# Performance work log

Measured on AMD Instinct MI355X. Metric: run time of the kernel, lower is better.

Reference implementation:

```python
import jax, jax.numpy as jnp
import numpy as np

N = 100000
MUL = 16


def _build_cg():
    # Real-basis Clebsch-Gordan (Wigner-3j-style) coefficients, shape (2l1+1, 2l2+1, 2lo+1),
    # each normalized to unit Frobenius norm per output component (e3nn component normalization).
    eps = np.zeros((3, 3, 3), np.float32)
    for a, b, c in [(0, 1, 2), (1, 2, 0), (2, 0, 1)]:
        eps[a, b, c] = 1.0
        eps[a, c, b] = -1.0
    s2 = np.float32(1.0 / np.sqrt(2.0))
    q = np.zeros((5, 3, 3), np.float32)  # l=2 real harmonics: xy, yz, 3z^2-r^2, xz, x^2-y^2
    q[0, 0, 1] = q[0, 1, 0] = s2
    q[1, 1, 2] = q[1, 2, 1] = s2
    q[2] = np.diag([-1.0, -1.0, 2.0]).astype(np.float32) / np.sqrt(6.0)
    q[3, 0, 2] = q[3, 2, 0] = s2
    q[4] = np.diag([1.0, -1.0, 0.0]).astype(np.float32) * s2
    cg000 = jnp.ones((1, 1, 1), jnp.float32)                                   # 0e x 0e -> 0e
    cg011 = jnp.asarray(np.eye(3, dtype=np.float32)[None])                      # 0e x 1o -> 1o
    cg110 = jnp.asarray((np.eye(3, dtype=np.float32) / np.sqrt(3.0))[:, :, None])  # 1o x 1o -> 0e
    cg111 = jnp.asarray(eps * s2)                                               # 1o x 1o -> 1e
    cg112 = jnp.asarray(np.transpose(q, (1, 2, 0)))                             # 1o x 1o -> 2e
    return cg000, cg011, cg110, cg111, cg112


def _path(x1, x2, cg, w, alpha):
    # 'uvw' tensor-product path: out[z,w,m] = alpha * sum_{u,v,i,j} x1[z,u,i] x2[z,v,j] cg[i,j,m] w[u,v,w]
    # Contraction order chosen to keep the largest intermediate at [z,u,w,j].
    t = jnp.einsum('zvj,uvw->zuwj', x2, w)
    s = jnp.einsum('zui,zuwj->zwij', x1, t)
    return alpha * jnp.einsum('zwij,ijm->zwm', s, cg)


def _tensor_square(x, w0, w1, w2, w3, w4):
    n = x.shape[0]
    x0 = x[:, :MUL].reshape(n, MUL, 1)       # 16x0e
    x1 = x[:, MUL:].reshape(n, MUL, 3)       # 16x1o
    cg000, cg011, cg110, cg111, cg112 = _build_cg()
    a2 = 1.0 / np.sqrt(MUL * MUL * 2.0)      # 0e output receives 2 paths
    a1 = 1.0 / np.sqrt(MUL * MUL * 1.0)
    o_0e = _path(x0, x0, cg000, w0, a2) + _path(x1, x1, cg110, w2, a2)
    o_1o = _path(x0, x1, cg011, w1, a1)
    o_1e = _path(x1, x1, cg111, w3, a1)
    o_2e = _path(x1, x1, cg112, w4, a1)
    return jnp.concatenate([o.reshape(n, -1) for o in (o_0e, o_1o, o_1e, o_2e)], axis=1)


def setup_inputs() -> dict:
    key = jax.random.key(0)
    kx, k0, k1, k2, k3, k4 = jax.random.split(key, 6)
    return {
        'x': jax.random.normal(kx, (N, MUL * 1 + MUL * 3), jnp.float32),
        'w0': jax.random.normal(k0, (MUL, MUL, MUL), jnp.float32),
        'w1': jax.random.normal(k1, (MUL, MUL, MUL), jnp.float32),
        'w2': jax.random.normal(k2, (MUL, MUL, MUL), jnp.float32),
        'w3': jax.random.normal(k3, (MUL, MUL, MUL), jnp.float32),
        'w4': jax.random.normal(k4, (MUL, MUL, MUL), jnp.float32),
    }


def reference(x, w0, w1, w2, w3, w4):
    return _tensor_square(x, w0, w1, w2, w3, w4)
```

## Files before the change

kernel.cpp:

```cpp
#include <hip/hip_runtime.h>
#include <hip/hip_bf16.h>

typedef __attribute__((ext_vector_type(8))) short short8;
typedef __attribute__((ext_vector_type(4))) float float4v;
typedef __attribute__((ext_vector_type(2))) float float2v;
typedef __attribute__((ext_vector_type(4))) unsigned uint4v;

#define S_A 0.04419417382415922f
#define S_B 0.025515518153991442f
#define S_C 0.0625f

static __device__ __forceinline__ unsigned pkbf(float a, float b) {
#if __has_builtin(__builtin_amdgcn_cvt_pk_bf16_f32)
    auto v = __builtin_amdgcn_cvt_pk_bf16_f32(a, b);
    return __builtin_bit_cast(unsigned, v);
#else
    unsigned ua = __builtin_bit_cast(unsigned, a);
    unsigned ub = __builtin_bit_cast(unsigned, b);
    ua += 0x7fffu + ((ua >> 16) & 1u);
    ub += 0x7fffu + ((ub >> 16) & 1u);
    return __builtin_amdgcn_perm(ub, ua, 0x07060302);
#endif
}

__global__ void wprep_kernel(const float* __restrict__ wA, const float* __restrict__ wB,
                             const float* __restrict__ wC, const float* __restrict__ wD,
                             const float* __restrict__ wE, unsigned short* __restrict__ wout)
{
    int e = blockIdx.x * 256 + threadIdx.x;
    if (e >= 5 * 4096) return;
    int p = e >> 12;
    int rem = e & 4095;
    const float* wp = (p == 0) ? wA : (p == 1) ? wB : (p == 2) ? wC : (p == 3) ? wD : wE;
    unsigned u = __builtin_bit_cast(unsigned, wp[rem]);
    u += 0x7fffu + ((u >> 16) & 1u);
    int k = rem >> 4, w = rem & 15;
    int c = k >> 5, kk = k & 31;
    int lane = ((kk >> 3) << 4) | w;
    int j = kk & 7;
    wout[(((c * 5 + p) * 64 + lane) << 3) | j] = (unsigned short)(u >> 16);
}

template<int G>
static __device__ __forceinline__ int pathof(int i) {
    if constexpr (G == 0) return (i == 0) ? 0 : (i == 1) ? 1 : 4;
    if constexpr (G == 1) return (i == 0) ? 2 : (i == 1) ? 3 : 4;
    return (i == 0) ? 3 : 4;
}

template<int G>
static __device__ __forceinline__ void run_group(
    const float* __restrict__ xr, int l, const short8* __restrict__ wbase,
    float* __restrict__ out, long long z0)
{
    const int r  = l & 15;
    const int g  = l >> 4;
    const int v0 = (g & 1) * 8;
    const int uo = g >> 1;

    float2v Xv[4], Yv[4], Zv[4];
    float2v A0v[4];
    {
        float b[24];
        #pragma unroll
        for (int q = 0; q < 6; q++)
            *(float4v*)&b[q * 4] = *(const float4v*)(xr + 16 + v0 * 3 + q * 4);
        #pragma unroll
        for (int t = 0; t < 4; t++) {
            Xv[t] = (float2v){b[6 * t + 0], b[6 * t + 3]};
            Yv[t] = (float2v){b[6 * t + 1], b[6 * t + 4]};
            Zv[t] = (float2v){b[6 * t + 2], b[6 * t + 5]};
        }
        if constexpr (G == 0) {
            float a[8];
            #pragma unroll
            for (int q = 0; q < 2; q++)
                *(float4v*)&a[q * 4] = *(const float4v*)(xr + v0 + q * 4);
            #pragma unroll
            for (int t = 0; t < 4; t++) A0v[t] = (float2v){a[2 * t], a[2 * t + 1]};
        }
    }

    constexpr int NS = (G == 1) ? 5 : 4;
    constexpr int NP = (G == 2) ? 2 : 3;

    float4v acc[NS];
    #pragma unroll
    for (int s = 0; s < NS; s++) acc[s] = (float4v){0.f, 0.f, 0.f, 0.f};

    #pragma unroll
    for (int c = 0; c < 8; c++) {
        short8 wf[NP];
        #pragma unroll
        for (int i = 0; i < NP; i++) wf[i] = wbase[(c * 5 + pathof<G>(i)) * 64 + l];

        const int u = c * 2 + uo;
        float u0 = 0.f, ux = 0.f, uy, uz;
        if constexpr (G != 2) u0 = xr[u];
        if constexpr (G != 1) ux = xr[16 + u * 3 + 0];
        uy = xr[16 + u * 3 + 1];
        uz = xr[16 + u * 3 + 2];

        unsigned fri[NS][4];
        #pragma unroll
        for (int t = 0; t < 4; t++) {
            const float2v X = Xv[t], Y = Yv[t], Z = Zv[t];
            if constexpr (G == 0) {
                float2v b0  = u0 * A0v[t];
                float2v p00 = ux * X, p11 = uy * Y, p22 = uz * Z;
                float2v t01 = p00 + p11;
                float2v b1  = t01 + p22;
                float2v b10 = 2.0f * p22 - t01;
                float2v b12 = p00 - p11;
                fri[0][t] = pkbf(b0.x, b0.y);
                fri[1][t] = pkbf(b1.x, b1.y);
                fri[2][t] = pkbf(b10.x, b10.y);
                fri[3][t] = pkbf(b12.x, b12.y);
            }
            if constexpr (G == 1) {
                float2v b2 = u0 * X, b3 = u0 * Y, b4 = u0 * Z;
                float2v p12 = uy * Z;
                float2v b5 = p12 - uz * Y;
                float2v b9 = p12 + uz * Y;
                fri[0][t] = pkbf(b2.x, b2.y);
                fri[1][t] = pkbf(b3.x, b3.y);
                fri[2][t] = pkbf(b4.x, b4.y);
                fri[3][t] = pkbf(b5.x, b5.y);
                fri[4][t] = pkbf(b9.x, b9.y);
            }
            if constexpr (G == 2) {
                float2v p01 = ux * Y;
                float2v b7  = p01 - uy * X;
                float2v b8  = p01 + uy * X;
                float2v p02 = ux * Z;
                float2v b6  = uz * X - p02;
                float2v b11 = p02 + uz * X;
                fri[0][t] = pkbf(b6.x, b6.y);
                fri[1][t] = pkbf(b7.x, b7.y);
                fri[2][t] = pkbf(b8.x, b8.y);
                fri[3][t] = pkbf(b11.x, b11.y);
            }
        }

        #pragma unroll
        for (int s = 0; s < NS; s++) {
            short8 frm = __builtin_bit_cast(short8, *(uint4v*)fri[s]);
            int wi;
            if constexpr (G == 0) wi = (s == 0) ? 0 : (s == 1) ? 1 : 2;
            if constexpr (G == 1) wi = (s <= 2) ? 0 : (s == 3) ? 1 : 2;
            if constexpr (G == 2) wi = (s <= 1) ? 0 : 1;
            acc[s] = __builtin_amdgcn_mfma_f32_16x16x32_bf16(frm, wf[wi], acc[s], 0, 0, 0);
        }
    }

    const int w = r;
    float* outp = out + (z0 + g * 4) * 192;
    #pragma unroll
    for (int reg = 0; reg < 4; reg++) {
        float* rowp = outp + reg * 192;
        if constexpr (G == 0) {
            rowp[w]               = S_A * acc[0][reg] + S_B * acc[1][reg];
            rowp[112 + w * 5 + 2] = S_B * acc[2][reg];
            rowp[112 + w * 5 + 4] = S_A * acc[3][reg];
        }
        if constexpr (G == 1) {
            rowp[16 + w * 3 + 0]  = S_C * acc[0][reg];
            rowp[16 + w * 3 + 1]  = S_C * acc[1][reg];
            rowp[16 + w * 3 + 2]  = S_C * acc[2][reg];
            rowp[64 + w * 3 + 0]  = S_A * acc[3][reg];
            rowp[112 + w * 5 + 1] = S_A * acc[4][reg];
        }
        if constexpr (G == 2) {
            rowp[64 + w * 3 + 1]  = S_A * acc[0][reg];
            rowp[64 + w * 3 + 2]  = S_A * acc[1][reg];
            rowp[112 + w * 5 + 0] = S_A * acc[2][reg];
            rowp[112 + w * 5 + 3] = S_A * acc[3][reg];
        }
    }
}

__global__ __launch_bounds__(384, 5)
void tsq_kernel(const float* __restrict__ x,
                const unsigned short* __restrict__ wfrag,
                float* __restrict__ out,
                int nrows)
{
    __shared__ __attribute__((aligned(16))) unsigned short wlds[5 * 4096];
    __shared__ __attribute__((aligned(16))) float xlds[32 * 68];

    const int tid = threadIdx.x;
    const long long z0 = (long long)blockIdx.x * 32;

    {
        const uint4v* src = (const uint4v*)wfrag;
        uint4v* dst = (uint4v*)wlds;
        #pragma unroll
        for (int rr = 0; rr < 6; rr++) dst[rr * 384 + tid] = src[rr * 384 + tid];
        if (tid < 256) dst[2304 + tid] = src[2304 + tid];
    }
    {
        const float* xg = x + z0 * 64;
        int f = tid * 4;
        int row = f >> 6, col = f & 63;
        float4v v = {0.f, 0.f, 0.f, 0.f};
        if (z0 + row < nrows) v = *(const float4v*)(xg + f);
        *(float4v*)&xlds[row * 68 + col] = v;
        if (tid < 128) {
            f = 1536 + tid * 4;
            row = f >> 6; col = f & 63;
            float4v v2 = {0.f, 0.f, 0.f, 0.f};
            if (z0 + row < nrows) v2 = *(const float4v*)(xg + f);
            *(float4v*)&xlds[row * 68 + col] = v2;
        }
    }
    __syncthreads();
    if (z0 >= nrows) return;

    const int wave = tid >> 6;
    const int l = tid & 63;
    const int tb = (wave >= 3) ? 1 : 0;
    const int grp = wave - tb * 3;
    const long long zb = z0 + tb * 16;
    if (zb >= nrows) return;

    const float* xr = &xlds[(tb * 16 + (l & 15)) * 68];
    const short8* wb = (const short8*)wlds;

    if      (grp == 0) run_group<0>(xr, l, wb, out, zb);
    else if (grp == 1) run_group<1>(xr, l, wb, out, zb);
    else               run_group<2>(xr, l, wb, out, zb);
}

extern "C" void kernel_launch(void* const* d_in, const int* in_sizes, int n_in,
                              void* d_out, int out_size, void* d_ws, size_t ws_size,
                              hipStream_t stream) {
    const float* x  = (const float*)d_in[0];
    const float* w0 = (const float*)d_in[1];
    const float* w1 = (const float*)d_in[2];
    const float* w2 = (const float*)d_in[3];
    const float* w3 = (const float*)d_in[4];
    const float* w4 = (const float*)d_in[5];
    float* out = (float*)d_out;
    unsigned short* wfrag = (unsigned short*)d_ws;
    (void)ws_size; (void)n_in; (void)out_size;

    const int nrows = in_sizes[0] / 64;
    const int nblocks = (nrows + 31) / 32;

    wprep_kernel<<<dim3(80), dim3(256), 0, stream>>>(w0, w2, w1, w3, w4, wfrag);
    tsq_kernel<<<dim3(nblocks), dim3(384), 0, stream>>>(x, wfrag, out, nrows);
}
```

Baseline: 141.4 us.

## Stage outputs in LDS for coalesced float4 stores and fold scales into weights

Results now go into a 32x192 LDS tile that reuses the x staging buffer, and the block writes it to global memory with coalesced float4 stores. Previously each lane did strided scalar global stores. The per-path normalization scales move into the weight prep kernel, leaving only one ratio multiply in the epilogue. Per-u x values are preloaded into registers before a barrier so the buffer can be overwritten. The cost is a larger LDS footprint, with launch-bounds occupancy dropped from 5 to 4, plus extra barriers and register pressure.

```diff
diff --git a/kernel.cpp b/kernel.cpp
--- a/kernel.cpp
+++ b/kernel.cpp
@@ -9,6 +9,7 @@
 #define S_A 0.04419417382415922f
 #define S_B 0.025515518153991442f
 #define S_C 0.0625f
+#define R_BA 0.5773502691896258f
 
 static __device__ __forceinline__ unsigned pkbf(float a, float b) {
 #if __has_builtin(__builtin_amdgcn_cvt_pk_bf16_f32)
@@ -32,7 +33,8 @@
     int p = e >> 12;
     int rem = e & 4095;
     const float* wp = (p == 0) ? wA : (p == 1) ? wB : (p == 2) ? wC : (p == 3) ? wD : wE;
-    unsigned u = __builtin_bit_cast(unsigned, wp[rem]);
+    const float scl = (p == 1) ? S_B : (p == 2) ? S_C : S_A;
+    unsigned u = __builtin_bit_cast(unsigned, scl * wp[rem]);
     u += 0x7fffu + ((u >> 16) & 1u);
     int k = rem >> 4, w = rem & 15;
     int c = k >> 5, kk = k & 31;
@@ -51,15 +53,14 @@
 template<int G>
 static __device__ __forceinline__ void run_group(
     const float* __restrict__ xr, int l, const short8* __restrict__ wbase,
-    float* __restrict__ out, long long z0)
+    float* __restrict__ outb, int rowbase)
 {
-    const int r  = l & 15;
+    const int w  = l & 15;
     const int g  = l >> 4;
     const int v0 = (g & 1) * 8;
     const int uo = g >> 1;
 
     float2v Xv[4], Yv[4], Zv[4];
-    float2v A0v[4];
     {
         float b[24];
         #pragma unroll
@@ -70,6 +71,18 @@
             Xv[t] = (float2v){b[6 * t + 0], b[6 * t + 3]};
             Yv[t] = (float2v){b[6 * t + 1], b[6 * t + 4]};
             Zv[t] = (float2v){b[6 * t + 2], b[6 * t + 5]};
+        }
+    }
+    float u0_[8], ux_[8], uy_[8], uz_[8];
+    float2v A0v[4];
+    {
+        const float* xu1 = xr + 16 + uo * 3;
+        #pragma unroll
+        for (int c = 0; c < 8; c++) {
+            if constexpr (G != 2) u0_[c] = xr[2 * c + uo];
+            if constexpr (G != 1) ux_[c] = xu1[6 * c + 0];
+            uy_[c] = xu1[6 * c + 1];
+            uz_[c] = xu1[6 * c + 2];
         }
         if constexpr (G == 0) {
             float a[8];
@@ -81,6 +94,8 @@
         }
     }
 
+    __syncthreads();
+
     constexpr int NS = (G == 1) ? 5 : 4;
     constexpr int NP = (G == 2) ? 2 : 3;
 
@@ -94,20 +109,13 @@
         #pragma unroll
         for (int i = 0; i < NP; i++) wf[i] = wbase[(c * 5 + pathof<G>(i)) * 64 + l];
 
-        const int u = c * 2 + uo;
-        float u0 = 0.f, ux = 0.f, uy, uz;
-        if constexpr (G != 2) u0 = xr[u];
-        if constexpr (G != 1) ux = xr[16 + u * 3 + 0];
-        uy = xr[16 + u * 3 + 1];
-        uz = xr[16 + u * 3 + 2];
-
         unsigned fri[NS][4];
         #pragma unroll
         for (int t = 0; t < 4; t++) {
             const float2v X = Xv[t], Y = Yv[t], Z = Zv[t];
             if constexpr (G == 0) {
-                float2v b0  = u0 * A0v[t];
-                float2v p00 = ux * X, p11 = uy * Y, p22 = uz * Z;
+                float2v b0  = u0_[c] * A0v[t];
+                float2v p00 = ux_[c] * X, p11 = uy_[c] * Y, p22 = uz_[c] * Z;
                 float2v t01 = p00 + p11;
                 float2v b1  = t01 + p22;
                 float2v b10 = 2.0f * p22 - t01;
@@ -118,10 +126,10 @@
                 fri[3][t] = pkbf(b12.x, b12.y);
             }
             if constexpr (G == 1) {
-                float2v b2 = u0 * X, b3 = u0 * Y, b4 = u0 * Z;
-                float2v p12 = uy * Z;
-                float2v b5 = p12 - uz * Y;
-                float2v b9 = p12 + uz * Y;
+                float2v b2 = u0_[c] * X, b3 = u0_[c] * Y, b4 = u0_[c] * Z;
+                float2v p12 = uy_[c] * Z;
+                float2v b5 = p12 - uz_[c] * Y;
+                float2v b9 = p12 + uz_[c] * Y;
                 fri[0][t] = pkbf(b2.x, b2.y);
                 fri[1][t] = pkbf(b3.x, b3.y);
                 fri[2][t] = pkbf(b4.x, b4.y);
@@ -129,12 +137,12 @@
                 fri[4][t] = pkbf(b9.x, b9.y);
             }
             if constexpr (G == 2) {
-                float2v p01 = ux * Y;
-                float2v b7  = p01 - uy * X;
-                float2v b8  = p01 + uy * X;
-                float2v p02 = ux * Z;
-                float2v b6  = uz * X - p02;
-                float2v b11 = p02 + uz * X;
+                float2v p01 = ux_[c] * Y;
+                float2v b7  = p01 - uy_[c] * X;
+                float2v b8  = p01 + uy_[c] * X;
+                float2v p02 = ux_[c] * Z;
+                float2v b6  = uz_[c] * X - p02;
+                float2v b11 = p02 + uz_[c] * X;
                 fri[0][t] = pkbf(b6.x, b6.y);
                 fri[1][t] = pkbf(b7.x, b7.y);
                 fri[2][t] = pkbf(b8.x, b8.y);
@@ -153,43 +161,43 @@
         }
     }
 
-    const int w = r;
-    float* outp = out + (z0 + g * 4) * 192;
+    const int rb0 = rowbase + g * 4;
     #pragma unroll
     for (int reg = 0; reg < 4; reg++) {
-        float* rowp = outp + reg * 192;
+        float* rp = outb + (rb0 + reg) * 192;
         if constexpr (G == 0) {
-            rowp[w]               = S_A * acc[0][reg] + S_B * acc[1][reg];
-            rowp[112 + w * 5 + 2] = S_B * acc[2][reg];
-            rowp[112 + w * 5 + 4] = S_A * acc[3][reg];
+            rp[w]               = acc[0][reg] + acc[1][reg];
+            rp[112 + w * 5 + 2] = R_BA * acc[2][reg];
+            rp[112 + w * 5 + 4] = acc[3][reg];
         }
         if constexpr (G == 1) {
-            rowp[16 + w * 3 + 0]  = S_C * acc[0][reg];
-            rowp[16 + w * 3 + 1]  = S_C * acc[1][reg];
-            rowp[16 + w * 3 + 2]  = S_C * acc[2][reg];
-            rowp[64 + w * 3 + 0]  = S_A * acc[3][reg];
-            rowp[112 + w * 5 + 1] = S_A * acc[4][reg];
+            rp[16 + w * 3 + 0]  = acc[0][reg];
+            rp[16 + w * 3 + 1]  = acc[1][reg];
+            rp[16 + w * 3 + 2]  = acc[2][reg];
+            rp[64 + w * 3 + 0]  = acc[3][reg];
+            rp[112 + w * 5 + 1] = acc[4][reg];
         }
         if constexpr (G == 2) {
-            rowp[64 + w * 3 + 1]  = S_A * acc[0][reg];
-            rowp[64 + w * 3 + 2]  = S_A * acc[1][reg];
-            rowp[112 + w * 5 + 0] = S_A * acc[2][reg];
-            rowp[112 + w * 5 + 3] = S_A * acc[3][reg];
-        }
-    }
-}
-
-__global__ __launch_bounds__(384, 5)
+            rp[64 + w * 3 + 1]  = acc[0][reg];
+            rp[64 + w * 3 + 2]  = acc[1][reg];
+            rp[112 + w * 5 + 0] = acc[2][reg];
+            rp[112 + w * 5 + 3] = acc[3][reg];
+        }
+    }
+}
+
+__global__ __launch_bounds__(384, 4)
 void tsq_kernel(const float* __restrict__ x,
                 const unsigned short* __restrict__ wfrag,
                 float* __restrict__ out,
                 int nrows)
 {
     __shared__ __attribute__((aligned(16))) unsigned short wlds[5 * 4096];
-    __shared__ __attribute__((aligned(16))) float xlds[32 * 68];
+    __shared__ __attribute__((aligned(16))) float xout[32 * 192];
 
     const int tid = threadIdx.x;
     const long long z0 = (long long)blockIdx.x * 32;
+    if (z0 >= nrows) return;
 
     {
         const uint4v* src = (const uint4v*)wfrag;
@@ -204,31 +212,41 @@
         int row = f >> 6, col = f & 63;
         float4v v = {0.f, 0.f, 0.f, 0.f};
         if (z0 + row < nrows) v = *(const float4v*)(xg + f);
-        *(float4v*)&xlds[row * 68 + col] = v;
+        *(float4v*)&xout[row * 68 + col] = v;
         if (tid < 128) {
             f = 1536 + tid * 4;
             row = f >> 6; col = f & 63;
             float4v v2 = {0.f, 0.f, 0.f, 0.f};
             if (z0 + row < nrows) v2 = *(const float4v*)(xg + f);
-            *(float4v*)&xlds[row * 68 + col] = v2;
+            *(float4v*)&xout[row * 68 + col] = v2;
         }
     }
     __syncthreads();
-    if (z0 >= nrows) return;
 
     const int wave = tid >> 6;
     const int l = tid & 63;
     const int tb = (wave >= 3) ? 1 : 0;
     const int grp = wave - tb * 3;
-    const long long zb = z0 + tb * 16;
-    if (zb >= nrows) return;
-
-    const float* xr = &xlds[(tb * 16 + (l & 15)) * 68];
+    const float* xr = &xout[(tb * 16 + (l & 15)) * 68];
     const short8* wb = (const short8*)wlds;
 
-    if      (grp == 0) run_group<0>(xr, l, wb, out, zb);
-    else if (grp == 1) run_group<1>(xr, l, wb, out, zb);
-    else               run_group<2>(xr, l, wb, out, zb);
+    if      (grp == 0) run_group<0>(xr, l, wb, xout, tb * 16);
+    else if (grp == 1) run_group<1>(xr, l, wb, xout, tb * 16);
+    else               run_group<2>(xr, l, wb, xout, tb * 16);
+
+    __syncthreads();
+    {
+        const int row0 = tid / 48;
+        const int cq   = tid - row0 * 48;
+        #pragma unroll
+        for (int k = 0; k < 4; k++) {
+            int rrow = row0 + k * 8;
+            long long grow = z0 + rrow;
+            if (grow < nrows)
+                *(float4v*)(out + grow * 192 + cq * 4) =
+                    *(const float4v*)&xout[rrow * 192 + cq * 4];
+        }
+    }
 }
 
 extern "C" void kernel_launch(void* const* d_in, const int* in_sizes, int n_in,
```

Measured after the change: 173.4 us. +22.7%, slower.
